# Kernel optimization log

Hardware: AMD Instinct MI355X
Metric: run time of the kernel (lower is better)

## Reference

```python
import jax, jax.numpy as jnp
import numpy as np

N_CIR, N_DIS, D, H = 585, 88, 128, 8
E_CC, E_DD = 20000, 3000
EPS = 1e-16


def _gcn(x, src, dst, ew, W, b, N):
    # PyG GCNConv: add self-loops (weight 1), symmetric normalization, x @ W, scatter-add, + bias
    loop = jnp.arange(N)
    s = jnp.concatenate([src, loop])
    d = jnp.concatenate([dst, loop])
    w = jnp.concatenate([ew, jnp.ones((N,), ew.dtype)])
    deg = jax.ops.segment_sum(w, d, num_segments=N)
    dinv = jnp.where(deg > 0, jax.lax.rsqrt(deg), 0.0)
    norm = dinv[s] * w * dinv[d]                      # [E+N]
    h = x @ W                                         # [N,D]
    out = jax.ops.segment_sum(h[s] * norm[:, None], d, num_segments=N)
    return out + b


def _gat(x, src, dst, ea, W, a_src, a_dst, a_edge, We, b, N):
    # PyG GATConv(heads=H, concat=False, edge_dim=1): self-loops with mean edge_attr fill,
    # leaky_relu attention logits, segment softmax over destination, mean over heads, + bias
    loop = jnp.arange(N)
    s = jnp.concatenate([src, loop])
    d = jnp.concatenate([dst, loop])
    ea = jnp.concatenate([ea, jnp.broadcast_to(ea.mean(0, keepdims=True), (N, ea.shape[1]))], 0)
    h = (x @ W).reshape(N, H, D)                      # [N,H,D]
    e = (ea @ We).reshape(-1, H, D)                   # [E+N,H,D]
    alpha = (h * a_src).sum(-1)[s] + (h * a_dst).sum(-1)[d] + (e * a_edge).sum(-1)
    alpha = jax.nn.leaky_relu(alpha, 0.2)             # [E+N,H]
    amax = jax.ops.segment_max(alpha, d, num_segments=N)
    ex = jnp.exp(alpha - amax[d])
    den = jax.ops.segment_sum(ex, d, num_segments=N)
    alpha = ex / (den[d] + EPS)
    out = jax.ops.segment_sum(h[s] * alpha[:, :, None], d, num_segments=N)  # [N,H,D]
    return out.mean(1) + b


def _branch(x, edges, mat, gw1, gb1, aw, asrc, adst, aedge, awe, ab, gw2, gb2, N):
    src, dst = edges[0], edges[1]
    ew = mat[src, dst]                                # gather edge weights from dense matrix
    f1 = jax.nn.relu(_gcn(x, src, dst, ew, gw1, gb1, N))
    att = jax.nn.relu(_gat(f1, src, dst, ew[:, None], aw, asrc, adst, aedge, awe, ab, N))
    f2 = jax.nn.relu(_gcn(att, src, dst, ew, gw2, gb2, N))
    return f1, f2


def _cnn(f1, f2, Wk, b):
    # Conv2d(2,256,(128,1)) over [1,2,128,N] == per-node GEMM over (2,128) then view/transpose
    Xv = jnp.stack([f1.T, f2.T])                      # [2,D,N]
    return jnp.einsum('ock,ckn->no', Wk[..., 0], Xv) + b  # [N,256]


def setup_inputs():
    ks = jax.random.split(jax.random.key(0), 24)
    rn = lambda i, sh, s=1.0: jax.random.normal(ks[i], sh, jnp.float32) * s
    w = 0.08  # ~glorot scale for fan-in 128
    return {
        'x_cir': rn(0, (N_CIR, D)),
        'x_dis': rn(1, (N_DIS, D)),
        'cc_matrix': jax.random.uniform(ks[2], (N_CIR, N_CIR), jnp.float32),
        'dd_matrix': jax.random.uniform(ks[3], (N_DIS, N_DIS), jnp.float32),
        'gcn_c1_w': rn(4, (D, D), w), 'gcn_c1_b': jnp.zeros((D,), jnp.float32),
        'gat_c_w': rn(5, (D, H * D), w), 'gat_c_asrc': rn(6, (H, D), w),
        'gat_c_adst': rn(7, (H, D), w), 'gat_c_aedge': rn(8, (H, D), w),
        'gat_c_we': rn(9, (1, H * D), w), 'gat_c_b': jnp.zeros((D,), jnp.float32),
        'gcn_c2_w': rn(10, (D, D), w), 'gcn_c2_b': jnp.zeros((D,), jnp.float32),
        'gcn_d1_w': rn(11, (D, D), w), 'gcn_d1_b': jnp.zeros((D,), jnp.float32),
        'gat_d_w': rn(12, (D, H * D), w), 'gat_d_asrc': rn(13, (H, D), w),
        'gat_d_adst': rn(14, (H, D), w), 'gat_d_aedge': rn(15, (H, D), w),
        'gat_d_we': rn(16, (1, H * D), w), 'gat_d_b': jnp.zeros((D,), jnp.float32),
        'gcn_d2_w': rn(17, (D, D), w), 'gcn_d2_b': jnp.zeros((D,), jnp.float32),
        'conv_c_w': rn(18, (256, 2, D, 1), w), 'conv_c_b': jnp.zeros((256,), jnp.float32),
        'conv_d_w': rn(19, (256, 2, D, 1), w), 'conv_d_b': jnp.zeros((256,), jnp.float32),
        'cc_edges': jax.random.randint(ks[20], (2, E_CC), 0, N_CIR),
        'dd_edges': jax.random.randint(ks[21], (2, E_DD), 0, N_DIS),
    }


def reference(x_cir, x_dis, cc_matrix, dd_matrix,
              gcn_c1_w, gcn_c1_b, gat_c_w, gat_c_asrc, gat_c_adst, gat_c_aedge, gat_c_we, gat_c_b,
              gcn_c2_w, gcn_c2_b,
              gcn_d1_w, gcn_d1_b, gat_d_w, gat_d_asrc, gat_d_adst, gat_d_aedge, gat_d_we, gat_d_b,
              gcn_d2_w, gcn_d2_b,
              conv_c_w, conv_c_b, conv_d_w, conv_d_b,
              cc_edges, dd_edges):
    c1, c2 = _branch(x_cir, cc_edges, cc_matrix, gcn_c1_w, gcn_c1_b, gat_c_w, gat_c_asrc,
                     gat_c_adst, gat_c_aedge, gat_c_we, gat_c_b, gcn_c2_w, gcn_c2_b, N_CIR)
    d1, d2 = _branch(x_dis, dd_edges, dd_matrix, gcn_d1_w, gcn_d1_b, gat_d_w, gat_d_asrc,
                     gat_d_adst, gat_d_aedge, gat_d_we, gat_d_b, gcn_d2_w, gcn_d2_b, N_DIS)
    cir_fea = _cnn(c1, c2, conv_c_w, conv_c_b)        # [585,256]
    dis_fea = _cnn(d1, d2, conv_d_w, conv_d_b)        # [88,256]
    return cir_fea @ dis_fea.T, cir_fea, dis_fea
```

## Files before the change

kernel.cpp:

```cpp
#include <hip/hip_runtime.h>

constexpr int NCIR = 585;
constexpr int NDIS = 88;
constexpr int NT   = NCIR + NDIS;
constexpr int DIM  = 128;
constexpr int NH   = 8;
constexpr int ECC  = 20000;
constexpr int EDD  = 3000;
constexpr int ET   = ECC + EDD;
constexpr int CO   = 256;
constexpr int CAP  = 256;
constexpr int F1C  = (NCIR + 3) / 4;
constexpr int F1D  = (NDIS + 3) / 4;
constexpr int NG   = F1C + F1D;
constexpr int CH   = 64;
constexpr int GBK  = (ET + 255) / 256;
constexpr int GEMB = (NT + 1) / 2;

struct P {
  const float *x_c, *x_d, *mat_c, *mat_d;
  const float *g1w_c, *g1b_c, *aw_c, *as_c, *ad_c, *ae_c, *we_c, *ab_c, *g2w_c, *g2b_c;
  const float *g1w_d, *g1b_d, *aw_d, *as_d, *ad_d, *ae_d, *we_d, *ab_d, *g2w_d, *g2b_d;
  const float *cw_c, *cb_c, *cw_d, *cb_d;
  const int *csrc, *cdst, *dsrc, *ddst;
  float *hs, *hd, *h, *f1, *hg, *fill_w, *psc, *psd, *wdeg;
  int *cnt, *fill_s;
  float *out_score, *out_cir, *out_dis;
};

__global__ __launch_bounds__(256) void k_gg(P p){
  __shared__ float r0[256], r1[256];
  int b = blockIdx.x, t = threadIdx.x;
  if (b < GBK){
    int e = b * 256 + t;
    float wc = 0.0f, wdv = 0.0f;
    if (e < ET){
      float w; int s, d;
      if (e < ECC){
        s = p.csrc[e]; d = p.cdst[e];
        w = p.mat_c[s * NCIR + d]; wc = w;
      } else {
        int el = e - ECC;
        s = NCIR + p.dsrc[el]; d = NCIR + p.ddst[el];
        w = p.mat_d[(s - NCIR) * NDIS + (d - NCIR)]; wdv = w;
      }
      int pos = atomicAdd(&p.cnt[d], 1);
      if (pos < CAP){
        p.fill_s[d * CAP + pos] = s;
        p.fill_w[d * CAP + pos] = w;
      }
      atomicAdd(&p.wdeg[d], w);
    }
    r0[t] = wc; r1[t] = wdv;
    __syncthreads();
    for (int st = 128; st; st >>= 1){
      if (t < st){ r0[t] += r0[t + st]; r1[t] += r1[t + st]; }
      __syncthreads();
    }
    if (t == 0){ p.psc[b] = r0[0]; p.psd[b] = r1[0]; }
  } else {
    int ub = (b - GBK) * 2;
    int n = t >> 7, k = t & 127;
    int u = ub + n;
    bool ok = u < NT;
    if (ok){
      int br = u >= NCIR;
      r0[n * DIM + k] = br ? p.x_d[(u - NCIR) * DIM + k] : p.x_c[u * DIM + k];
    }
    __syncthreads();
    if (ok){
      const float* W = (u >= NCIR) ? p.g1w_d : p.g1w_c;
      float acc = 0.0f;
      #pragma unroll 8
      for (int c = 0; c < DIM; ++c) acc += r0[n * DIM + c] * W[c * DIM + k];
      p.h[u * DIM + k] = acc;
    }
  }
}

__global__ __launch_bounds__(256) void k_aggproj(P p){
  __shared__ float a_sh4[4][DIM];
  __shared__ float wred[4][8];
  int b = blockIdx.x, t = threadIdx.x;
  int ng = b >> 2, ct = b & 3;
  int base, count, br;
  if (ng < F1C){ base = ng * 4; count = min(4, NCIR - base); br = 0; }
  else { base = NCIR + (ng - F1C) * 4; count = 4; br = 1; }
  const float* B1 = br ? p.g1b_d : p.g1b_c;
  int n2 = t >> 7, k = t & 127;
  for (int r = 0; r < 2; ++r){
    int nn = n2 + r * 2;
    float v = 0.0f;
    if (nn < count){
      int u = base + nn;
      float dvu = rsqrtf(1.0f + p.wdeg[u]);
      float acc = B1[k] + p.h[u * DIM + k] * dvu * dvu;
      int deg = min(p.cnt[u], CAP);
      const int*   fs = p.fill_s + u * CAP;
      const float* fw = p.fill_w + u * CAP;
      for (int j = 0; j < deg; ++j){
        int s = fs[j];
        acc += p.h[s * DIM + k] * (rsqrtf(1.0f + p.wdeg[s]) * fw[j] * dvu);
      }
      if (ct == 0) p.f1[u * DIM + k] = acc;
      v = fmaxf(acc, 0.0f);
    }
    a_sh4[nn][k] = v;
  }
  __syncthreads();
  const float* W = (br ? p.aw_d : p.aw_c) + ct * 256 + t;
  float acc[4] = {0.f, 0.f, 0.f, 0.f};
  #pragma unroll 4
  for (int c = 0; c < DIM; ++c){
    float w = W[c * 1024];
    acc[0] += a_sh4[0][c] * w; acc[1] += a_sh4[1][c] * w;
    acc[2] += a_sh4[2][c] * w; acc[3] += a_sh4[3][c] * w;
  }
  int col = ct * 256 + t;
  for (int n = 0; n < count; ++n)
    p.hg[(size_t)(base + n) * 1024 + col] = acc[n];
  const float* As = br ? p.as_d : p.as_c;
  const float* Ad = br ? p.ad_d : p.ad_c;
  float av = As[col], dw = Ad[col];
  int w = t >> 6;
  #pragma unroll
  for (int n = 0; n < 4; ++n){
    float sdot = acc[n] * av, ddot = acc[n] * dw;
    #pragma unroll
    for (int off = 32; off; off >>= 1){
      sdot += __shfl_down(sdot, off, 64);
      ddot += __shfl_down(ddot, off, 64);
    }
    if ((t & 63) == 0){ wred[w][n * 2] = sdot; wred[w][n * 2 + 1] = ddot; }
  }
  __syncthreads();
  if (t < 16){
    int g = t >> 3, v = t & 7, n = v >> 1, isd = v & 1;
    if (n < count){
      float sum = wred[g * 2][v] + wred[g * 2 + 1][v];
      float* dst = isd ? p.hd : p.hs;
      dst[(base + n) * NH + ct * 2 + g] = sum;
    }
  }
}

__global__ __launch_bounds__(256) void k_att(P p){
  __shared__ float den_sh[NH], hd_sh[NH], inv_sh[NH], wself_sh[NH], wd_sh[NH];
  __shared__ float slw_sh;
  __shared__ float alpha_sh[CH * NH];
  __shared__ int   s_sh[CH];
  __shared__ float a2[2][DIM], attv[DIM], part[2][DIM];
  int d = blockIdx.x, t = threadIdx.x;
  int g = t >> 7, k = t & 127;
  int br = d >= NCIR;
  int wv = t >> 6, lane = t & 63;
  if (t < NH){ den_sh[t] = 0.0f; hd_sh[t] = p.hd[d * NH + t]; }
  if (wv == 0){
    const float* ps = br ? p.psd : p.psc;
    float v = (lane < GBK ? ps[lane] : 0.0f) + (lane + 64 < GBK ? ps[lane + 64] : 0.0f);
    #pragma unroll
    for (int off = 32; off; off >>= 1) v += __shfl_down(v, off, 64);
    if (lane == 0) slw_sh = v / (br ? (float)EDD : (float)ECC);
  }
  if (wv >= 2){
    const float* We = br ? p.we_d : p.we_c;
    const float* Ae = br ? p.ae_d : p.ae_c;
    for (int q = 0; q < 4; ++q){
      int hh = (wv - 2) * 4 + q;
      float v = We[hh * DIM + lane] * Ae[hh * DIM + lane]
              + We[hh * DIM + 64 + lane] * Ae[hh * DIM + 64 + lane];
      #pragma unroll
      for (int off = 32; off; off >>= 1) v += __shfl_down(v, off, 64);
      if (lane == 0) wd_sh[hh] = v;
    }
  }
  __syncthreads();
  int beg = d * CAP;
  int deg = min(p.cnt[d], CAP);
  int end = beg + deg;
  float slw = slw_sh;
  for (int idx = t; idx < deg * NH; idx += 256){
    int j = beg + (idx >> 3), hh = idx & 7;
    int s = p.fill_s[j];
    float a = p.hs[s * NH + hh] + hd_sh[hh] + p.fill_w[j] * wd_sh[hh];
    a = a > 0.0f ? a : 0.2f * a;
    atomicAdd(&den_sh[hh], expf(a));
  }
  __syncthreads();
  if (t < NH){
    float a = p.hs[d * NH + t] + hd_sh[t] + slw * wd_sh[t];
    a = a > 0.0f ? a : 0.2f * a;
    float ex = expf(a);
    float inv = 1.0f / (den_sh[t] + ex + 1e-16f) * 0.125f;
    inv_sh[t] = inv;
    wself_sh[t] = ex * inv;
  }
  __syncthreads();
  float acc = 0.0f;
  if (g == 0){
    acc = (br ? p.ab_d : p.ab_c)[k];
    const float* r = p.hg + (size_t)d * 1024;
    #pragma unroll
    for (int hh = 0; hh < NH; ++hh) acc += wself_sh[hh] * r[hh * DIM + k];
  }
  for (int j0 = beg; j0 < end; j0 += CH){
    int m = min(CH, end - j0);
    for (int idx = t; idx < m * NH; idx += 256){
      int jj = idx >> 3, hh = idx & 7;
      int j = j0 + jj;
      int s = p.fill_s[j];
      float a = p.hs[s * NH + hh] + hd_sh[hh] + p.fill_w[j] * wd_sh[hh];
      a = a > 0.0f ? a : 0.2f * a;
      alpha_sh[idx] = expf(a) * inv_sh[hh];
    }
    if (t < m) s_sh[t] = p.fill_s[j0 + t];
    __syncthreads();
    for (int jj = g; jj < m; jj += 2){
      const float* r = p.hg + (size_t)s_sh[jj] * 1024;
      #pragma unroll
      for (int hh = 0; hh < NH; ++hh) acc += alpha_sh[jj * NH + hh] * r[hh * DIM + k];
    }
    __syncthreads();
  }
  a2[g][k] = acc;
  __syncthreads();
  if (g == 0) attv[k] = fmaxf(a2[0][k] + a2[1][k], 0.0f);
  __syncthreads();
  const float* W = br ? p.g2w_d : p.g2w_c;
  float h2 = 0.0f;
  #pragma unroll 8
  for (int c = g * 64; c < g * 64 + 64; ++c) h2 += attv[c] * W[c * DIM + k];
  part[g][k] = h2;
  __syncthreads();
  if (g == 0) p.h[d * DIM + k] = part[0][k] + part[1][k];
}

__global__ __launch_bounds__(256) void k_fuse2(P p){
  __shared__ float s12[4][2 * DIM];
  int b = blockIdx.x, o = threadIdx.x;
  int gbase, count, br; float* out;
  if (b < F1C){ gbase = b * 4; count = min(4, NCIR - gbase); br = 0;
                out = p.out_cir + (size_t)gbase * CO; }
  else { int lb = (b - F1C) * 4; gbase = NCIR + lb; count = 4; br = 1;
         out = p.out_dis + (size_t)lb * CO; }
  const float* B2 = br ? p.g2b_d : p.g2b_c;
  int n2 = o >> 7, k = o & 127;
  for (int r = 0; r < 2; ++r){
    int nn = n2 + r * 2;
    float v1 = 0.0f, v2 = 0.0f;
    if (nn < count){
      int u = gbase + nn;
      float dvu = rsqrtf(1.0f + p.wdeg[u]);
      float acc = B2[k] + p.h[u * DIM + k] * dvu * dvu;
      int deg = min(p.cnt[u], CAP);
      const int*   fs = p.fill_s + u * CAP;
      const float* fw = p.fill_w + u * CAP;
      for (int j = 0; j < deg; ++j){
        int s = fs[j];
        acc += p.h[s * DIM + k] * (rsqrtf(1.0f + p.wdeg[s]) * fw[j] * dvu);
      }
      v2 = fmaxf(acc, 0.0f);
      v1 = fmaxf(p.f1[u * DIM + k], 0.0f);
    }
    s12[nn][k] = v1;
    s12[nn][DIM + k] = v2;
  }
  __syncthreads();
  const float* W = (br ? p.cw_d : p.cw_c) + o * 2 * DIM;
  float bv = (br ? p.cb_d : p.cb_c)[o];
  float a0 = bv, a1 = bv, a2 = bv, a3 = bv;
  #pragma unroll 4
  for (int q = 0; q < 2 * DIM; ++q){
    float wv = W[q];
    a0 += s12[0][q] * wv; a1 += s12[1][q] * wv;
    a2 += s12[2][q] * wv; a3 += s12[3][q] * wv;
  }
  if (0 < count) out[0 * CO + o] = a0;
  if (1 < count) out[1 * CO + o] = a1;
  if (2 < count) out[2 * CO + o] = a2;
  if (3 < count) out[3 * CO + o] = a3;
}

__global__ void k_final(P p){
  __shared__ float ci[CO];
  int i = blockIdx.x, j = threadIdx.x;
  ci[j]       = p.out_cir[i * CO + j];
  ci[DIM + j] = p.out_cir[i * CO + DIM + j];
  __syncthreads();
  if (j < NDIS){
    const float* dr = p.out_dis + j * CO;
    float acc = 0.0f;
    #pragma unroll 8
    for (int q = 0; q < CO; ++q) acc += ci[q] * dr[q];
    p.out_score[i * NDIS + j] = acc;
  }
}

extern "C" void kernel_launch(void* const* d_in, const int* in_sizes, int n_in,
                              void* d_out, int out_size, void* d_ws, size_t ws_size,
                              hipStream_t stream){
  P p;
  typedef const float* F;
  p.x_c   = (F)d_in[0];  p.x_d   = (F)d_in[1];
  p.mat_c = (F)d_in[2];  p.mat_d = (F)d_in[3];
  p.g1w_c = (F)d_in[4];  p.g1b_c = (F)d_in[5];
  p.aw_c  = (F)d_in[6];  p.as_c  = (F)d_in[7];  p.ad_c = (F)d_in[8];
  p.ae_c  = (F)d_in[9];  p.we_c  = (F)d_in[10]; p.ab_c = (F)d_in[11];
  p.g2w_c = (F)d_in[12]; p.g2b_c = (F)d_in[13];
  p.g1w_d = (F)d_in[14]; p.g1b_d = (F)d_in[15];
  p.aw_d  = (F)d_in[16]; p.as_d  = (F)d_in[17]; p.ad_d = (F)d_in[18];
  p.ae_d  = (F)d_in[19]; p.we_d  = (F)d_in[20]; p.ab_d = (F)d_in[21];
  p.g2w_d = (F)d_in[22]; p.g2b_d = (F)d_in[23];
  p.cw_c  = (F)d_in[24]; p.cb_c  = (F)d_in[25];
  p.cw_d  = (F)d_in[26]; p.cb_d  = (F)d_in[27];
  const int* cc_edges = (const int*)d_in[28];
  const int* dd_edges = (const int*)d_in[29];
  p.csrc = cc_edges;  p.cdst = cc_edges + ECC;
  p.dsrc = dd_edges;  p.ddst = dd_edges + EDD;

  float* out = (float*)d_out;
  p.out_score = out;
  p.out_cir   = out + NCIR * NDIS;
  p.out_dis   = p.out_cir + NCIR * CO;

  float* w = (float*)d_ws;
  auto alloc = [&](size_t n){ float* q = w; w += n; return q; };
  p.wdeg   = alloc(676);
  p.cnt    = (int*)alloc(676);
  p.psc    = alloc(92);
  p.psd    = alloc(92);
  p.hs     = alloc((size_t)NT * NH);
  p.hd     = alloc((size_t)NT * NH);
  p.h      = alloc((size_t)NT * DIM);
  p.f1     = alloc((size_t)NT * DIM);
  p.hg     = alloc((size_t)NT * 1024);
  p.fill_w = alloc((size_t)NT * CAP);
  p.fill_s = (int*)alloc((size_t)NT * CAP);

  hipMemsetAsync(p.wdeg, 0, 2 * 676 * sizeof(float), stream);
  k_gg     <<<GBK + GEMB, 256, 0, stream>>>(p);
  k_aggproj<<<NG * 4,     256, 0, stream>>>(p);
  k_att    <<<NT,         256, 0, stream>>>(p);
  k_fuse2  <<<F1C + F1D,  256, 0, stream>>>(p);
  k_final  <<<NCIR,       DIM, 0, stream>>>(p);
}
```

Measured before the change: 222.0 us.

## Split GCN aggregation out of projection and stage neighbor lists in shared memory

The first GCN aggregation moves out of k_aggproj into a new per-node kernel (k_agg1), so it is no longer recomputed four times, once per column tile. In k_att and k_fuse2, neighbor indices and normalized weights are now loaded once into shared memory. k_att also caches its exp values instead of recomputing them in a second chunked pass. This adds a kernel launch and a round trip of f1 through global memory, and uses more shared memory per block, which can lower occupancy.

```diff
diff --git a/kernel.cpp b/kernel.cpp
--- a/kernel.cpp
+++ b/kernel.cpp
@@ -13,7 +13,6 @@
 constexpr int F1C  = (NCIR + 3) / 4;
 constexpr int F1D  = (NDIS + 3) / 4;
 constexpr int NG   = F1C + F1D;
-constexpr int CH   = 64;
 constexpr int GBK  = (ET + 255) / 256;
 constexpr int GEMB = (NT + 1) / 2;
 
@@ -78,34 +77,38 @@
   }
 }
 
-__global__ __launch_bounds__(256) void k_aggproj(P p){
-  __shared__ float a_sh4[4][DIM];
+__global__ __launch_bounds__(128) void k_agg1(P p){
+  __shared__ int   s_l[CAP];
+  __shared__ float nrm_l[CAP];
+  int d = blockIdx.x, k = threadIdx.x;
+  int br = d >= NCIR;
+  float dvu = rsqrtf(1.0f + p.wdeg[d]);
+  int deg = min(p.cnt[d], CAP);
+  for (int j = k; j < deg; j += 128){
+    int s = p.fill_s[d * CAP + j];
+    s_l[j] = s;
+    nrm_l[j] = rsqrtf(1.0f + p.wdeg[s]) * p.fill_w[d * CAP + j] * dvu;
+  }
+  __syncthreads();
+  const float* B1 = br ? p.g1b_d : p.g1b_c;
+  float acc = B1[k] + p.h[d * DIM + k] * dvu * dvu;
+  #pragma unroll 4
+  for (int j = 0; j < deg; ++j)
+    acc += p.h[s_l[j] * DIM + k] * nrm_l[j];
+  p.f1[d * DIM + k] = acc;
+}
+
+__global__ __launch_bounds__(256) void k_proj(P p){
+  __shared__ float a_sh[4][DIM];
   __shared__ float wred[4][8];
   int b = blockIdx.x, t = threadIdx.x;
   int ng = b >> 2, ct = b & 3;
   int base, count, br;
   if (ng < F1C){ base = ng * 4; count = min(4, NCIR - base); br = 0; }
   else { base = NCIR + (ng - F1C) * 4; count = 4; br = 1; }
-  const float* B1 = br ? p.g1b_d : p.g1b_c;
-  int n2 = t >> 7, k = t & 127;
-  for (int r = 0; r < 2; ++r){
-    int nn = n2 + r * 2;
-    float v = 0.0f;
-    if (nn < count){
-      int u = base + nn;
-      float dvu = rsqrtf(1.0f + p.wdeg[u]);
-      float acc = B1[k] + p.h[u * DIM + k] * dvu * dvu;
-      int deg = min(p.cnt[u], CAP);
-      const int*   fs = p.fill_s + u * CAP;
-      const float* fw = p.fill_w + u * CAP;
-      for (int j = 0; j < deg; ++j){
-        int s = fs[j];
-        acc += p.h[s * DIM + k] * (rsqrtf(1.0f + p.wdeg[s]) * fw[j] * dvu);
-      }
-      if (ct == 0) p.f1[u * DIM + k] = acc;
-      v = fmaxf(acc, 0.0f);
-    }
-    a_sh4[nn][k] = v;
+  for (int i = 0; i < 2; ++i){
+    int idx = t + i * 256, n = idx >> 7, c = idx & 127;
+    a_sh[n][c] = (n < count) ? fmaxf(p.f1[(base + n) * DIM + c], 0.0f) : 0.0f;
   }
   __syncthreads();
   const float* W = (br ? p.aw_d : p.aw_c) + ct * 256 + t;
@@ -113,8 +116,8 @@
   #pragma unroll 4
   for (int c = 0; c < DIM; ++c){
     float w = W[c * 1024];
-    acc[0] += a_sh4[0][c] * w; acc[1] += a_sh4[1][c] * w;
-    acc[2] += a_sh4[2][c] * w; acc[3] += a_sh4[3][c] * w;
+    acc[0] += a_sh[0][c] * w; acc[1] += a_sh[1][c] * w;
+    acc[2] += a_sh[2][c] * w; acc[3] += a_sh[3][c] * w;
   }
   int col = ct * 256 + t;
   for (int n = 0; n < count; ++n)
@@ -147,8 +150,9 @@
 __global__ __launch_bounds__(256) void k_att(P p){
   __shared__ float den_sh[NH], hd_sh[NH], inv_sh[NH], wself_sh[NH], wd_sh[NH];
   __shared__ float slw_sh;
-  __shared__ float alpha_sh[CH * NH];
-  __shared__ int   s_sh[CH];
+  __shared__ int   s_all[CAP];
+  __shared__ float w_all[CAP];
+  __shared__ float alpha_all[CAP * NH];
   __shared__ float a2[2][DIM], attv[DIM], part[2][DIM];
   int d = blockIdx.x, t = threadIdx.x;
   int g = t >> 7, k = t & 127;
@@ -174,27 +178,33 @@
       if (lane == 0) wd_sh[hh] = v;
     }
   }
-  __syncthreads();
-  int beg = d * CAP;
   int deg = min(p.cnt[d], CAP);
-  int end = beg + deg;
-  float slw = slw_sh;
+  for (int j = t; j < deg; j += 256){
+    s_all[j] = p.fill_s[d * CAP + j];
+    w_all[j] = p.fill_w[d * CAP + j];
+  }
+  __syncthreads();
   for (int idx = t; idx < deg * NH; idx += 256){
-    int j = beg + (idx >> 3), hh = idx & 7;
-    int s = p.fill_s[j];
-    float a = p.hs[s * NH + hh] + hd_sh[hh] + p.fill_w[j] * wd_sh[hh];
+    int j = idx >> 3, hh = idx & 7;
+    int s = s_all[j];
+    float a = p.hs[s * NH + hh] + hd_sh[hh] + w_all[j] * wd_sh[hh];
     a = a > 0.0f ? a : 0.2f * a;
-    atomicAdd(&den_sh[hh], expf(a));
+    float ex = expf(a);
+    alpha_all[idx] = ex;
+    atomicAdd(&den_sh[hh], ex);
   }
   __syncthreads();
   if (t < NH){
-    float a = p.hs[d * NH + t] + hd_sh[t] + slw * wd_sh[t];
+    float a = p.hs[d * NH + t] + hd_sh[t] + slw_sh * wd_sh[t];
     a = a > 0.0f ? a : 0.2f * a;
     float ex = expf(a);
     float inv = 1.0f / (den_sh[t] + ex + 1e-16f) * 0.125f;
     inv_sh[t] = inv;
     wself_sh[t] = ex * inv;
   }
+  __syncthreads();
+  for (int idx = t; idx < deg * NH; idx += 256)
+    alpha_all[idx] *= inv_sh[idx & 7];
   __syncthreads();
   float acc = 0.0f;
   if (g == 0){
@@ -203,24 +213,11 @@
     #pragma unroll
     for (int hh = 0; hh < NH; ++hh) acc += wself_sh[hh] * r[hh * DIM + k];
   }
-  for (int j0 = beg; j0 < end; j0 += CH){
-    int m = min(CH, end - j0);
-    for (int idx = t; idx < m * NH; idx += 256){
-      int jj = idx >> 3, hh = idx & 7;
-      int j = j0 + jj;
-      int s = p.fill_s[j];
-      float a = p.hs[s * NH + hh] + hd_sh[hh] + p.fill_w[j] * wd_sh[hh];
-      a = a > 0.0f ? a : 0.2f * a;
-      alpha_sh[idx] = expf(a) * inv_sh[hh];
-    }
-    if (t < m) s_sh[t] = p.fill_s[j0 + t];
-    __syncthreads();
-    for (int jj = g; jj < m; jj += 2){
-      const float* r = p.hg + (size_t)s_sh[jj] * 1024;
-      #pragma unroll
-      for (int hh = 0; hh < NH; ++hh) acc += alpha_sh[jj * NH + hh] * r[hh * DIM + k];
-    }
-    __syncthreads();
+  for (int jj = g; jj < deg; jj += 2){
+    const float* r = p.hg + (size_t)s_all[jj] * 1024;
+    const float* al = alpha_all + jj * NH;
+    #pragma unroll
+    for (int hh = 0; hh < NH; ++hh) acc += al[hh] * r[hh * DIM + k];
   }
   a2[g][k] = acc;
   __syncthreads();
@@ -237,12 +234,34 @@
 
 __global__ __launch_bounds__(256) void k_fuse2(P p){
   __shared__ float s12[4][2 * DIM];
+  __shared__ int   deg4[4];
+  __shared__ float dv4[4];
+  __shared__ int   s4[4][CAP];
+  __shared__ float nrm4[4][CAP];
   int b = blockIdx.x, o = threadIdx.x;
   int gbase, count, br; float* out;
   if (b < F1C){ gbase = b * 4; count = min(4, NCIR - gbase); br = 0;
                 out = p.out_cir + (size_t)gbase * CO; }
   else { int lb = (b - F1C) * 4; gbase = NCIR + lb; count = 4; br = 1;
          out = p.out_dis + (size_t)lb * CO; }
+  if (o < 4){
+    if (o < count){
+      int u = gbase + o;
+      deg4[o] = min(p.cnt[u], CAP);
+      dv4[o]  = rsqrtf(1.0f + p.wdeg[u]);
+    } else deg4[o] = 0;
+  }
+  __syncthreads();
+  for (int idx = o; idx < 4 * CAP; idx += 256){
+    int nn = idx >> 8, j = idx & (CAP - 1);
+    if (j < deg4[nn]){
+      int u = gbase + nn;
+      int s = p.fill_s[u * CAP + j];
+      s4[nn][j] = s;
+      nrm4[nn][j] = rsqrtf(1.0f + p.wdeg[s]) * p.fill_w[u * CAP + j] * dv4[nn];
+    }
+  }
+  __syncthreads();
   const float* B2 = br ? p.g2b_d : p.g2b_c;
   int n2 = o >> 7, k = o & 127;
   for (int r = 0; r < 2; ++r){
@@ -250,15 +269,12 @@
     float v1 = 0.0f, v2 = 0.0f;
     if (nn < count){
       int u = gbase + nn;
-      float dvu = rsqrtf(1.0f + p.wdeg[u]);
+      float dvu = dv4[nn];
       float acc = B2[k] + p.h[u * DIM + k] * dvu * dvu;
-      int deg = min(p.cnt[u], CAP);
-      const int*   fs = p.fill_s + u * CAP;
-      const float* fw = p.fill_w + u * CAP;
-      for (int j = 0; j < deg; ++j){
-        int s = fs[j];
-        acc += p.h[s * DIM + k] * (rsqrtf(1.0f + p.wdeg[s]) * fw[j] * dvu);
-      }
+      int deg = deg4[nn];
+      #pragma unroll 4
+      for (int j = 0; j < deg; ++j)
+        acc += p.h[s4[nn][j] * DIM + k] * nrm4[nn][j];
       v2 = fmaxf(acc, 0.0f);
       v1 = fmaxf(p.f1[u * DIM + k], 0.0f);
     }
@@ -338,9 +354,10 @@
   p.fill_s = (int*)alloc((size_t)NT * CAP);
 
   hipMemsetAsync(p.wdeg, 0, 2 * 676 * sizeof(float), stream);
-  k_gg     <<<GBK + GEMB, 256, 0, stream>>>(p);
-  k_aggproj<<<NG * 4,     256, 0, stream>>>(p);
-  k_att    <<<NT,         256, 0, stream>>>(p);
-  k_fuse2  <<<F1C + F1D,  256, 0, stream>>>(p);
-  k_final  <<<NCIR,       DIM, 0, stream>>>(p);
-}
+  k_gg    <<<GBK + GEMB, 256, 0, stream>>>(p);
+  k_agg1  <<<NT,         128, 0, stream>>>(p);
+  k_proj  <<<NG * 4,     256, 0, stream>>>(p);
+  k_att   <<<NT,         256, 0, stream>>>(p);
+  k_fuse2 <<<F1C + F1D,  256, 0, stream>>>(p);
+  k_final <<<NCIR,       DIM, 0, stream>>>(p);
+}
```

Result: faster. 193.9 us (-12.7%).
